# Kernel tuning notes

Measured on AMD Instinct MI355X. Metric: run time of the kernel, lower is better.

Reference implementation:

```python
import jax, jax.numpy as jnp
import numpy as np

HID = 5120
NH = 40
HD = HID // NH  # 128
S = 2048        # q_len == model_max_length (prefill)


def setup_inputs() -> dict:
    key = jax.random.key(0)
    k1, k2, k3 = jax.random.split(key, 3)
    hidden_states = jax.random.normal(k1, (1, S, HID), dtype=jnp.float32)
    W_pack_w = jax.random.normal(k2, (3 * HID, HID), dtype=jnp.float32) * 0.02
    o_proj_w = jax.random.normal(k3, (HID, HID), dtype=jnp.float32) * 0.02
    k_cache = jnp.zeros((1, NH, S, HD), dtype=jnp.float32)
    v_cache = jnp.zeros((1, NH, S, HD), dtype=jnp.float32)
    input_pos = jnp.arange(S, dtype=jnp.int32)
    # persistent causal mask [bsz, 1, max_len, max_len]; True = attend
    attention_mask = jnp.tril(jnp.ones((S, S), dtype=bool))[None, None, :, :]
    return {
        "hidden_states": hidden_states,
        "W_pack_w": W_pack_w,
        "o_proj_w": o_proj_w,
        "k_cache": k_cache,
        "v_cache": v_cache,
        "input_pos": input_pos,
        "attention_mask": attention_mask,
    }


def reference(hidden_states, W_pack_w, o_proj_w, k_cache, v_cache, input_pos, attention_mask):
    bsz, q_len, _ = hidden_states.shape
    # fused QKV projection (torch Linear weight is [out, in])
    proj = jnp.einsum("bsh,oh->bso", hidden_states, W_pack_w)  # [1,S,3H]
    q, k, v = jnp.split(proj, 3, axis=-1)
    def to_heads(t):
        return t.reshape(bsz, q_len, NH, HD).transpose(0, 2, 1, 3)  # [1,NH,S,HD]
    q, k, v = to_heads(q), to_heads(k), to_heads(v)
    # KV-cache scatter update at input_pos
    k_cache = k_cache.at[:, :, input_pos, :].set(k)
    v_cache = v_cache.at[:, :, input_pos, :].set(v)
    # s_len = input_pos[-1] + 1 == S (full prefill, static shape)
    keys = k_cache  # [1,NH,S,HD]
    vals = v_cache
    mask = attention_mask[:, :, input_pos, :]  # [1,1,S,S]
    scale = 1.0 / jnp.sqrt(jnp.asarray(HD, dtype=q.dtype))
    scores = jnp.einsum("bhqd,bhkd->bhqk", q, keys) * scale  # [1,NH,S,S]
    neg = jnp.finfo(scores.dtype).min
    scores = jnp.where(mask, scores, neg)
    attn = jax.nn.softmax(scores, axis=-1)
    out = jnp.einsum("bhqk,bhkd->bhqd", attn, vals)  # [1,NH,S,HD]
    out = out.transpose(0, 2, 1, 3).reshape(bsz, q_len, HID)
    return jnp.einsum("bsh,oh->bso", out, o_proj_w)
```

## Files before the change

### kernel.cpp

```cpp
#include <hip/hip_runtime.h>

#define S 2048
#define HID 5120
#define NH 40
#define HD 128

typedef unsigned short u16;
typedef __attribute__((ext_vector_type(8))) short short8;
typedef __attribute__((ext_vector_type(4))) float f32x4;

__device__ __forceinline__ u16 f2bf(float f) {
  union { float f; unsigned u; } x; x.f = f;
  unsigned r = x.u + 0x7fffu + ((x.u >> 16) & 1u);
  return (u16)(r >> 16);
}

__device__ __forceinline__ void gl_lds16(const void* g, void* l) {
  __builtin_amdgcn_global_load_lds((__attribute__((address_space(1))) void*)g,
                                   (__attribute__((address_space(3))) void*)l,
                                   16, 0, 0);
}

__global__ __launch_bounds__(256) void cvt4(const float4* __restrict__ s,
                                            ushort4* __restrict__ d, int n4) {
  int i = blockIdx.x * 256 + threadIdx.x;
  if (i >= n4) return;
  float4 v = s[i];
  ushort4 o;
  o.x = f2bf(v.x); o.y = f2bf(v.y); o.z = f2bf(v.z); o.w = f2bf(v.w);
  d[i] = o;
}

__global__ __launch_bounds__(512, 2) void gemm256(
    const u16* __restrict__ A, const u16* __restrict__ B,
    int N, int K,
    float* __restrict__ C,
    u16* __restrict__ qb, u16* __restrict__ kb, u16* __restrict__ vtb,
    int mode)
{
  __shared__ __align__(16) u16 As[2][16384];
  __shared__ __align__(16) u16 Bs[2][16384];

  const int tid = threadIdx.x;
  const int lane = tid & 63;
  const int wave = tid >> 6;
  const int wm = wave >> 2, wn = wave & 3;
  const int l16 = lane & 15, quad = lane >> 4;

  const int xcd = blockIdx.x & 7;
  const int j = blockIdx.x >> 3;
  const int ntile = xcd + ((j >> 3) << 3);
  if (ntile >= (N >> 8)) return;
  const int m0 = (j & 7) << 8;
  const int n0 = ntile << 8;

  const int srow = wave * 8 + (lane >> 3);
  const int scb  = (lane & 7) ^ ((lane >> 3) & 7);
  const u16* Abase = A + (long)(m0 + srow) * K + scb * 8;
  const u16* Bbase = B + (long)(n0 + srow) * K + scb * 8;
  u16* AsW = &As[0][0] + wave * 512;
  u16* BsW = &Bs[0][0] + wave * 512;

  const u16* ArBase = &As[0][0] + (wm * 128 + l16) * 64;
  const u16* BrBase = &Bs[0][0] + (wn * 64 + l16) * 64;
  const int acb0 = ((quad) ^ (l16 & 7)) * 8;
  const int acb1 = ((4 + quad) ^ (l16 & 7)) * 8;

  f32x4 acc[8][4];
#pragma unroll
  for (int i = 0; i < 8; ++i)
#pragma unroll
    for (int j2 = 0; j2 < 4; ++j2) acc[i][j2] = (f32x4){0.f, 0.f, 0.f, 0.f};

  short8 aP[2][2], aN[2][2], brg[4][2];

  const int nt = K >> 6;

#define STAGE_A(bufi, h, kt) do {                                         \
    const u16* g_ = Abase + (long)(h) * 128 * K + (long)(kt) * 64;        \
    gl_lds16(g_,           AsW + (bufi) * 16384 + (h) * 8192);            \
    gl_lds16(g_ + 64L * K, AsW + (bufi) * 16384 + (h) * 8192 + 4096);     \
  } while (0)

#define STAGE_B(bufi, h, kt) do {                                         \
    const u16* g_ = Bbase + (long)(h) * 128 * K + (long)(kt) * 64;        \
    gl_lds16(g_,           BsW + (bufi) * 16384 + (h) * 8192);            \
    gl_lds16(g_ + 64L * K, BsW + (bufi) * 16384 + (h) * 8192 + 4096);     \
  } while (0)

#define RD_A(dst, bufi, q) do {                                           \
    const u16* p_ = ArBase + (bufi) * 16384 + (q) * 2048;                 \
    dst[0][0] = *(const short8*)(p_ + acb0);                              \
    dst[0][1] = *(const short8*)(p_ + acb1);                              \
    dst[1][0] = *(const short8*)(p_ + 1024 + acb0);                       \
    dst[1][1] = *(const short8*)(p_ + 1024 + acb1);                       \
  } while (0)

#define RD_B(bufi) do {                                                   \
    const u16* p_ = BrBase + (bufi) * 16384;                              \
    brg[0][0] = *(const short8*)(p_ + acb0);                              \
    brg[0][1] = *(const short8*)(p_ + acb1);                              \
    brg[1][0] = *(const short8*)(p_ + 1024 + acb0);                       \
    brg[1][1] = *(const short8*)(p_ + 1024 + acb1);                       \
    brg[2][0] = *(const short8*)(p_ + 2048 + acb0);                       \
    brg[2][1] = *(const short8*)(p_ + 2048 + acb1);                       \
    brg[3][0] = *(const short8*)(p_ + 3072 + acb0);                       \
    brg[3][1] = *(const short8*)(p_ + 3072 + acb1);                       \
  } while (0)

#define MFMA1(mi, jj, ar) do {                                                            \
    acc[mi][jj] = __builtin_amdgcn_mfma_f32_16x16x32_bf16(ar[0], brg[jj][0], acc[mi][jj], 0, 0, 0); \
    acc[mi][jj] = __builtin_amdgcn_mfma_f32_16x16x32_bf16(ar[1], brg[jj][1], acc[mi][jj], 0, 0, 0); \
  } while (0)

#define MFMA_Q(q, a) do {                                                 \
    MFMA1((q)*2 + 0, 0, a[0]); MFMA1((q)*2 + 0, 1, a[0]);                 \
    MFMA1((q)*2 + 0, 2, a[0]); MFMA1((q)*2 + 0, 3, a[0]);                 \
    MFMA1((q)*2 + 1, 0, a[1]); MFMA1((q)*2 + 1, 1, a[1]);                 \
    MFMA1((q)*2 + 1, 2, a[1]); MFMA1((q)*2 + 1, 3, a[1]);                 \
  } while (0)

#define ASM_VMCNT(n) asm volatile("s_waitcnt vmcnt(" #n ")" ::: "memory")
#define BAR() __builtin_amdgcn_s_barrier()
#define PRIO1 __builtin_amdgcn_s_setprio(1)
#define PRIO0 __builtin_amdgcn_s_setprio(0)

#define KGROUP(S1, S2, VMN) do {                                          \
    const int bi = t & 1, bn = bi ^ 1;                                    \
                                                                 \
    RD_B(bi);                                                             \
    RD_A(aN, bi, 1);                                                      \
    if (S1) STAGE_A(bn, 1, t + 1);                                        \
    BAR();                                                                \
    PRIO1; MFMA_Q(0, aP); PRIO0;                                          \
    BAR();                                                                \
                                                                 \
    RD_A(aP, bi, 2);                                                      \
    if (S2) STAGE_B(bi, 0, t + 2);                                        \
    BAR();                                                                \
    PRIO1; MFMA_Q(1, aN); PRIO0;                                          \
    BAR();                                                                \
                                                                 \
    RD_A(aN, bi, 3);                                                      \
    if (S2) STAGE_B(bi, 1, t + 2);                                        \
    BAR();                                                                \
    PRIO1; MFMA_Q(2, aP); PRIO0;                                          \
    BAR();                                                                \
                                                                 \
    ASM_VMCNT(VMN);                                                       \
    __builtin_amdgcn_sched_barrier(0);                                    \
    BAR();                                                                \
    if (S1) RD_A(aP, bn, 0);                                              \
    PRIO1; MFMA_Q(3, aN); PRIO0;                                          \
    if (S2) STAGE_A(bi, 0, t + 2);                                        \
    BAR();                                                                \
  } while (0)

  STAGE_A(0, 0, 0); STAGE_A(0, 1, 0);
  STAGE_B(0, 0, 0); STAGE_B(0, 1, 0);
  STAGE_B(1, 0, 1); STAGE_B(1, 1, 1);
  ASM_VMCNT(4);
  __builtin_amdgcn_sched_barrier(0);
  BAR();
  STAGE_A(1, 0, 1);
  RD_A(aP, 0, 0);

  for (int t = 0; t < nt - 2; ++t) { KGROUP(1, 1, 4); }
  { int t = nt - 2; KGROUP(1, 0, 0); }
  { int t = nt - 1; KGROUP(0, 0, 0); }

  if (mode == 0) {
#pragma unroll
    for (int mi = 0; mi < 8; ++mi)
#pragma unroll
      for (int r = 0; r < 4; ++r) {
        int row = m0 + wm * 128 + mi * 16 + quad * 4 + r;
        float* cp = C + (long)row * N + n0 + wn * 64 + l16;
#pragma unroll
        for (int jj = 0; jj < 4; ++jj) cp[jj * 16] = acc[mi][jj][r];
      }
  } else {
    const int which = n0 / HID;
    const int hbase = (n0 % HID) >> 7;
    const float qs = 0.08838834764831845f;
#pragma unroll
    for (int mi = 0; mi < 8; ++mi)
#pragma unroll
      for (int jj = 0; jj < 4; ++jj) {
        int colIn = wn * 64 + jj * 16 + l16;
        int head = hbase + (colIn >> 7);
        int d = colIn & 127;
#pragma unroll
        for (int r = 0; r < 4; ++r) {
          int sI = m0 + wm * 128 + mi * 16 + quad * 4 + r;
          float v = acc[mi][jj][r];
          if (which == 0)      qb[((long)head * S + sI) * HD + d] = f2bf(v * qs);
          else if (which == 1) kb[((long)head * S + sI) * HD + d] = f2bf(v);
          else                 vtb[((long)head * HD + d) * S + sI] = f2bf(v);
        }
      }
  }

#undef STAGE_A
#undef STAGE_B
#undef RD_A
#undef RD_B
#undef MFMA1
#undef MFMA_Q
#undef ASM_VMCNT
#undef BAR
#undef PRIO1
#undef PRIO0
#undef KGROUP
}

__global__ __launch_bounds__(256) void attn_kernel(
    const u16* __restrict__ qg, const u16* __restrict__ kg,
    const u16* __restrict__ vg, u16* __restrict__ og)
{
  __shared__ __align__(16) u16 Qs[64 * 128];
  __shared__ __align__(16) u16 Ks[64 * 128];
  __shared__ __align__(16) u16 Vs[128 * 64];
  __shared__ float redm[2][64];
  __shared__ float reds[2][64];

  const int tid = threadIdx.x;
  const int lane = tid & 63;
  const int wid = tid >> 6;
  const int wm = wid >> 1, wn = wid & 1;
  const int l16 = lane & 15, quad = lane >> 4;
  const int qt = blockIdx.x;
  const int h = blockIdx.y;
  const int q0 = qt * 64;

  u16* Ps = Ks;

  {
    const u16* src = qg + ((long)h * S + q0) * HD;
#pragma unroll
    for (int cc = 0; cc < 4; ++cc) {
      int c = wid * 4 + cc;
      int row = c * 4 + (lane >> 4);
      int cb = (lane & 15) ^ (row & 7);
      gl_lds16(src + row * HD + cb * 8, &Qs[c * 512]);
    }
  }

  f32x4 acc_o[2][4];
#pragma unroll
  for (int i = 0; i < 2; ++i)
#pragma unroll
    for (int j = 0; j < 4; ++j)
      acc_o[i][j] = (f32x4){0.f, 0.f, 0.f, 0.f};
  float m_st[2][4], l_st[2][4];
#pragma unroll
  for (int i = 0; i < 2; ++i)
#pragma unroll
    for (int r = 0; r < 4; ++r) { m_st[i][r] = -1e30f; l_st[i][r] = 0.f; }

  for (int kt = 0; kt <= qt; ++kt) {
    __syncthreads();
    {
      const u16* ksrc = kg + ((long)h * S + kt * 64) * HD;
#pragma unroll
      for (int cc = 0; cc < 4; ++cc) {
        int c = wid * 4 + cc;
        int row = c * 4 + (lane >> 4);
        int cb = (lane & 15) ^ (row & 7);
        gl_lds16(ksrc + row * HD + cb * 8, &Ks[c * 512]);
      }
      const u16* vsrc = vg + (long)h * HD * S + kt * 64;
#pragma unroll
      for (int cc = 0; cc < 4; ++cc) {
        int c = wid * 4 + cc;
        int row = c * 8 + (lane >> 3);
        int cb = (lane & 7) ^ (row & 7);
        gl_lds16(vsrc + (long)row * S + cb * 8, &Vs[c * 512]);
      }
    }
    __syncthreads();

    f32x4 acc_s[2][2];
#pragma unroll
    for (int i = 0; i < 2; ++i)
#pragma unroll
      for (int j = 0; j < 2; ++j)
        acc_s[i][j] = (f32x4){0.f, 0.f, 0.f, 0.f};
#pragma unroll
    for (int kk = 0; kk < 128; kk += 32) {
      short8 aq[2], bk[2];
      const int cb0 = (kk >> 3) + quad;
#pragma unroll
      for (int i = 0; i < 2; ++i) {
        int row = wm * 32 + i * 16 + l16;
        aq[i] = *(const short8*)&Qs[row * 128 + (cb0 ^ (row & 7)) * 8];
      }
#pragma unroll
      for (int j = 0; j < 2; ++j) {
        int row = wn * 32 + j * 16 + l16;
        bk[j] = *(const short8*)&Ks[row * 128 + (cb0 ^ (row & 7)) * 8];
      }
#pragma unroll
      for (int i = 0; i < 2; ++i)
#pragma unroll
        for (int j = 0; j < 2; ++j)
          acc_s[i][j] = __builtin_amdgcn_mfma_f32_16x16x32_bf16(aq[i], bk[j], acc_s[i][j], 0, 0, 0);
    }

    if (kt == qt) {
#pragma unroll
      for (int i = 0; i < 2; ++i)
#pragma unroll
        for (int j = 0; j < 2; ++j)
#pragma unroll
          for (int r = 0; r < 4; ++r) {
            int row = wm * 32 + i * 16 + quad * 4 + r;
            int col = wn * 32 + j * 16 + l16;
            if (col > row) acc_s[i][j][r] = -1e30f;
          }
    }

#pragma unroll
    for (int i = 0; i < 2; ++i)
#pragma unroll
      for (int r = 0; r < 4; ++r) {
        float v = fmaxf(acc_s[i][0][r], acc_s[i][1][r]);
        v = fmaxf(v, __shfl_xor(v, 1));
        v = fmaxf(v, __shfl_xor(v, 2));
        v = fmaxf(v, __shfl_xor(v, 4));
        v = fmaxf(v, __shfl_xor(v, 8));
        if (l16 == 0) redm[wn][wm * 32 + i * 16 + quad * 4 + r] = v;
      }
    __syncthreads();

    float alpha[2][4], mnew[2][4], psum[2][4];
#pragma unroll
    for (int i = 0; i < 2; ++i)
#pragma unroll
      for (int r = 0; r < 4; ++r) {
        int row = wm * 32 + i * 16 + quad * 4 + r;
        float mn = fmaxf(m_st[i][r], fmaxf(redm[0][row], redm[1][row]));
        mnew[i][r] = mn;
        alpha[i][r] = __expf(m_st[i][r] - mn);
        m_st[i][r] = mn;
        psum[i][r] = 0.f;
      }
#pragma unroll
    for (int i = 0; i < 2; ++i)
#pragma unroll
      for (int j = 0; j < 2; ++j)
#pragma unroll
        for (int r = 0; r < 4; ++r) {
          int row = wm * 32 + i * 16 + quad * 4 + r;
          int col = wn * 32 + j * 16 + l16;
          float p = __expf(acc_s[i][j][r] - mnew[i][r]);
          psum[i][r] += p;
          Ps[row * 64 + ((col >> 3) ^ (row & 7)) * 8 + (col & 7)] = f2bf(p);
        }
#pragma unroll
    for (int i = 0; i < 2; ++i)
#pragma unroll
      for (int r = 0; r < 4; ++r) {
        float v = psum[i][r];
        v += __shfl_xor(v, 1);
        v += __shfl_xor(v, 2);
        v += __shfl_xor(v, 4);
        v += __shfl_xor(v, 8);
        if (l16 == 0) reds[wn][wm * 32 + i * 16 + quad * 4 + r] = v;
      }
    __syncthreads();

#pragma unroll
    for (int i = 0; i < 2; ++i)
#pragma unroll
      for (int r = 0; r < 4; ++r) {
        int row = wm * 32 + i * 16 + quad * 4 + r;
        l_st[i][r] = alpha[i][r] * l_st[i][r] + reds[0][row] + reds[1][row];
#pragma unroll
        for (int j = 0; j < 4; ++j)
          acc_o[i][j][r] *= alpha[i][r];
      }
#pragma unroll
    for (int kk = 0; kk < 64; kk += 32) {
      short8 ap[2], bv[4];
      const int cb0 = (kk >> 3) + quad;
#pragma unroll
      for (int i = 0; i < 2; ++i) {
        int m = wm * 32 + i * 16 + l16;
        ap[i] = *(const short8*)&Ps[m * 64 + (cb0 ^ (m & 7)) * 8];
      }
#pragma unroll
      for (int j = 0; j < 4; ++j) {
        int n = wn * 64 + j * 16 + l16;
        bv[j] = *(const short8*)&Vs[n * 64 + (cb0 ^ (n & 7)) * 8];
      }
#pragma unroll
      for (int i = 0; i < 2; ++i)
#pragma unroll
        for (int j = 0; j < 4; ++j)
          acc_o[i][j] = __builtin_amdgcn_mfma_f32_16x16x32_bf16(ap[i], bv[j], acc_o[i][j], 0, 0, 0);
    }
  }

#pragma unroll
  for (int i = 0; i < 2; ++i)
#pragma unroll
    for (int r = 0; r < 4; ++r) {
      int row = wm * 32 + i * 16 + quad * 4 + r;
      float inv = 1.f / l_st[i][r];
#pragma unroll
      for (int j = 0; j < 4; ++j) {
        int d = wn * 64 + j * 16 + l16;
        og[(long)(q0 + row) * HID + h * HD + d] = f2bf(acc_o[i][j][r] * inv);
      }
    }
}

extern "C" void kernel_launch(void* const* d_in, const int* in_sizes, int n_in,
                              void* d_out, int out_size, void* d_ws, size_t ws_size,
                              hipStream_t stream) {
  const float* hs = (const float*)d_in[0];
  const float* wp = (const float*)d_in[1];
  const float* wo = (const float*)d_in[2];
  float* out = (float*)d_out;
  char* ws = (char*)d_ws;

  u16* hsb = (u16*)(ws);
  u16* wpb = (u16*)(ws + 20971520L);
  u16* wob = (u16*)(ws + 178257920L);
  u16* qb  = (u16*)(ws + 230686720L);
  u16* kb  = (u16*)(ws + 251658240L);
  u16* vtb = (u16*)(ws + 272629760L);
  u16* aob = (u16*)(ws + 293601280L);
  if (ws_size < 314572800UL) return;

  cvt4<<<10240, 256, 0, stream>>>((const float4*)hs, (ushort4*)hsb, 2621440);
  cvt4<<<76800, 256, 0, stream>>>((const float4*)wp, (ushort4*)wpb, 19660800);
  cvt4<<<25600, 256, 0, stream>>>((const float4*)wo, (ushort4*)wob, 6553600);

  gemm256<<<dim3(512), dim3(512), 0, stream>>>(hsb, wpb, 15360, 5120,
                                               nullptr, qb, kb, vtb, 1);
  attn_kernel<<<dim3(32, 40), 256, 0, stream>>>(qb, kb, vtb, aob);
  gemm256<<<dim3(192), dim3(512), 0, stream>>>(aob, wob, 5120, 5120,
                                               out, nullptr, nullptr, nullptr, 0);
}
```

Measured before the change: 1.541 ms.

## Restructure attention to 128-row tiles with per-wave rows and double-buffered K/V

The attention kernel moves from 64-query tiles on 4 waves to 128-query tiles on 8 waves. Each wave owns 16 full query rows, so the row max and row sum now reduce inside the wave and the shared-memory reductions and two barriers per step are gone. Q fragments are held in registers, K/V tiles are double-buffered in one shared pool with prefetch two tiles ahead, and blocks start with the longest causal rows first to balance load. The risks are higher register and LDS pressure per block, and the loop has no explicit wait for the prefetched K/V loads, so correctness depends on the barrier draining them.

```diff
diff --git a/kernel.cpp b/kernel.cpp
--- a/kernel.cpp
+++ b/kernel.cpp
@@ -214,206 +214,188 @@
 #undef KGROUP
 }
 
-__global__ __launch_bounds__(256) void attn_kernel(
+__device__ __forceinline__ void stage_kv(const u16* __restrict__ ksrc0,
+                                         const u16* __restrict__ vsrc0,
+                                         u16* pool, int buf, int t,
+                                         int wave, int lane) {
+  const u16* ks_ = ksrc0 + (long)t * 64 * HD;
+  const u16* vs_ = vsrc0 + t * 64;
+#pragma unroll
+  for (int cc = 0; cc < 2; ++cc) {
+    int c = wave * 2 + cc;
+    int row = c * 4 + (lane >> 4);
+    int cb = (lane & 15) ^ (row & 7);
+    gl_lds16(ks_ + row * HD + cb * 8, &pool[buf * 8192 + c * 512]);
+  }
+#pragma unroll
+  for (int cc = 0; cc < 2; ++cc) {
+    int c = wave * 2 + cc;
+    int row = c * 8 + (lane >> 3);
+    int cb = (lane & 7) ^ (row & 7);
+    gl_lds16(vs_ + (long)row * S + cb * 8, &pool[16384 + buf * 8192 + c * 512]);
+  }
+}
+
+__global__ __launch_bounds__(512, 4) void attn_kernel(
     const u16* __restrict__ qg, const u16* __restrict__ kg,
     const u16* __restrict__ vg, u16* __restrict__ og)
 {
-  __shared__ __align__(16) u16 Qs[64 * 128];
-  __shared__ __align__(16) u16 Ks[64 * 128];
-  __shared__ __align__(16) u16 Vs[128 * 64];
-  __shared__ float redm[2][64];
-  __shared__ float reds[2][64];
+  __shared__ __align__(16) u16 pool[40960];
 
   const int tid = threadIdx.x;
   const int lane = tid & 63;
-  const int wid = tid >> 6;
-  const int wm = wid >> 1, wn = wid & 1;
+  const int wave = tid >> 6;
   const int l16 = lane & 15, quad = lane >> 4;
-  const int qt = blockIdx.x;
+  const int qt = (int)gridDim.x - 1 - (int)blockIdx.x;
   const int h = blockIdx.y;
-  const int q0 = qt * 64;
-
-  u16* Ps = Ks;
+  const int q0 = qt * 128;
+  const int nkt = 2 * qt + 2;
+
+  u16* Qs = pool;
+  u16* Ps = pool + 32768;
 
   {
     const u16* src = qg + ((long)h * S + q0) * HD;
 #pragma unroll
     for (int cc = 0; cc < 4; ++cc) {
-      int c = wid * 4 + cc;
+      int c = wave * 4 + cc;
       int row = c * 4 + (lane >> 4);
       int cb = (lane & 15) ^ (row & 7);
       gl_lds16(src + row * HD + cb * 8, &Qs[c * 512]);
     }
   }
-
-  f32x4 acc_o[2][4];
-#pragma unroll
-  for (int i = 0; i < 2; ++i)
-#pragma unroll
-    for (int j = 0; j < 4; ++j)
-      acc_o[i][j] = (f32x4){0.f, 0.f, 0.f, 0.f};
-  float m_st[2][4], l_st[2][4];
-#pragma unroll
-  for (int i = 0; i < 2; ++i)
-#pragma unroll
-    for (int r = 0; r < 4; ++r) { m_st[i][r] = -1e30f; l_st[i][r] = 0.f; }
-
-  for (int kt = 0; kt <= qt; ++kt) {
-    __syncthreads();
-    {
-      const u16* ksrc = kg + ((long)h * S + kt * 64) * HD;
-#pragma unroll
-      for (int cc = 0; cc < 4; ++cc) {
-        int c = wid * 4 + cc;
-        int row = c * 4 + (lane >> 4);
-        int cb = (lane & 15) ^ (row & 7);
-        gl_lds16(ksrc + row * HD + cb * 8, &Ks[c * 512]);
+  __syncthreads();
+  short8 aq[4];
+  {
+    const int row = wave * 16 + l16;
+    const u16* qr = &Qs[row * 128];
+    const int sw = row & 7;
+#pragma unroll
+    for (int ks = 0; ks < 4; ++ks)
+      aq[ks] = *(const short8*)(qr + ((ks * 4 + quad) ^ sw) * 8);
+  }
+  __syncthreads();
+
+  const u16* ksrc0 = kg + (long)h * S * HD;
+  const u16* vsrc0 = vg + (long)h * HD * S;
+
+  stage_kv(ksrc0, vsrc0, pool, 0, 0, wave, lane);
+  stage_kv(ksrc0, vsrc0, pool, 1, 1, wave, lane);
+  asm volatile("s_waitcnt vmcnt(4)" ::: "memory");
+  __builtin_amdgcn_sched_barrier(0);
+  __builtin_amdgcn_s_barrier();
+
+  f32x4 acc_o[8];
+#pragma unroll
+  for (int j2 = 0; j2 < 8; ++j2) acc_o[j2] = (f32x4){0.f, 0.f, 0.f, 0.f};
+  float m_st[4], l_st[4];
+#pragma unroll
+  for (int r = 0; r < 4; ++r) { m_st[r] = -1e30f; l_st[r] = 0.f; }
+
+  const int prow = wave * 16 + quad * 4;
+  const int rowA = wave * 16 + l16;
+  const int swA = rowA & 7;
+
+  for (int t = 0; t < nkt; ++t) {
+    const int cur = t & 1;
+    const u16* Ks = &pool[cur * 8192];
+    const u16* Vs = &pool[16384 + cur * 8192];
+
+    f32x4 acc_s[4];
+#pragma unroll
+    for (int j2 = 0; j2 < 4; ++j2) acc_s[j2] = (f32x4){0.f, 0.f, 0.f, 0.f};
+#pragma unroll
+    for (int ks = 0; ks < 4; ++ks) {
+      short8 bk[4];
+#pragma unroll
+      for (int j2 = 0; j2 < 4; ++j2) {
+        int row = j2 * 16 + l16;
+        bk[j2] = *(const short8*)&Ks[row * 128 + (((ks * 4 + quad) ^ (row & 7)) * 8)];
       }
-      const u16* vsrc = vg + (long)h * HD * S + kt * 64;
-#pragma unroll
-      for (int cc = 0; cc < 4; ++cc) {
-        int c = wid * 4 + cc;
-        int row = c * 8 + (lane >> 3);
-        int cb = (lane & 7) ^ (row & 7);
-        gl_lds16(vsrc + (long)row * S + cb * 8, &Vs[c * 512]);
+      __builtin_amdgcn_s_setprio(1);
+#pragma unroll
+      for (int j2 = 0; j2 < 4; ++j2)
+        acc_s[j2] = __builtin_amdgcn_mfma_f32_16x16x32_bf16(aq[ks], bk[j2], acc_s[j2], 0, 0, 0);
+      __builtin_amdgcn_s_setprio(0);
+    }
+
+    if (t >= nkt - 2) {
+#pragma unroll
+      for (int j2 = 0; j2 < 4; ++j2)
+#pragma unroll
+        for (int r = 0; r < 4; ++r) {
+          int row_abs = q0 + prow + r;
+          int col_abs = t * 64 + j2 * 16 + l16;
+          if (col_abs > row_abs) acc_s[j2][r] = -1e30f;
+        }
+    }
+
+    float mnew[4], alpha[4], psum[4];
+#pragma unroll
+    for (int r = 0; r < 4; ++r) {
+      float v = fmaxf(fmaxf(acc_s[0][r], acc_s[1][r]), fmaxf(acc_s[2][r], acc_s[3][r]));
+      v = fmaxf(v, __shfl_xor(v, 1));
+      v = fmaxf(v, __shfl_xor(v, 2));
+      v = fmaxf(v, __shfl_xor(v, 4));
+      v = fmaxf(v, __shfl_xor(v, 8));
+      float mn = fmaxf(m_st[r], v);
+      mnew[r] = mn;
+      alpha[r] = __expf(m_st[r] - mn);
+      m_st[r] = mn;
+      psum[r] = 0.f;
+    }
+#pragma unroll
+    for (int j2 = 0; j2 < 4; ++j2)
+#pragma unroll
+      for (int r = 0; r < 4; ++r) {
+        int row = prow + r;
+        int colL = j2 * 16 + l16;
+        float p = __expf(acc_s[j2][r] - mnew[r]);
+        psum[r] += p;
+        Ps[row * 64 + (((colL >> 3) ^ (row & 7)) * 8) + (colL & 7)] = f2bf(p);
       }
-    }
-    __syncthreads();
-
-    f32x4 acc_s[2][2];
-#pragma unroll
-    for (int i = 0; i < 2; ++i)
-#pragma unroll
-      for (int j = 0; j < 2; ++j)
-        acc_s[i][j] = (f32x4){0.f, 0.f, 0.f, 0.f};
-#pragma unroll
-    for (int kk = 0; kk < 128; kk += 32) {
-      short8 aq[2], bk[2];
-      const int cb0 = (kk >> 3) + quad;
-#pragma unroll
-      for (int i = 0; i < 2; ++i) {
-        int row = wm * 32 + i * 16 + l16;
-        aq[i] = *(const short8*)&Qs[row * 128 + (cb0 ^ (row & 7)) * 8];
+#pragma unroll
+    for (int r = 0; r < 4; ++r) {
+      float v = psum[r];
+      v += __shfl_xor(v, 1);
+      v += __shfl_xor(v, 2);
+      v += __shfl_xor(v, 4);
+      v += __shfl_xor(v, 8);
+      l_st[r] = alpha[r] * l_st[r] + v;
+#pragma unroll
+      for (int j2 = 0; j2 < 8; ++j2) acc_o[j2][r] *= alpha[r];
+    }
+
+#pragma unroll
+    for (int ks = 0; ks < 2; ++ks) {
+      short8 ap = *(const short8*)&Ps[rowA * 64 + (((ks * 4 + quad) ^ swA) * 8)];
+      short8 bv[8];
+#pragma unroll
+      for (int j2 = 0; j2 < 8; ++j2) {
+        int d = j2 * 16 + l16;
+        bv[j2] = *(const short8*)&Vs[d * 64 + (((ks * 4 + quad) ^ (d & 7)) * 8)];
       }
-#pragma unroll
-      for (int j = 0; j < 2; ++j) {
-        int row = wn * 32 + j * 16 + l16;
-        bk[j] = *(const short8*)&Ks[row * 128 + (cb0 ^ (row & 7)) * 8];
-      }
-#pragma unroll
-      for (int i = 0; i < 2; ++i)
-#pragma unroll
-        for (int j = 0; j < 2; ++j)
-          acc_s[i][j] = __builtin_amdgcn_mfma_f32_16x16x32_bf16(aq[i], bk[j], acc_s[i][j], 0, 0, 0);
-    }
-
-    if (kt == qt) {
-#pragma unroll
-      for (int i = 0; i < 2; ++i)
-#pragma unroll
-        for (int j = 0; j < 2; ++j)
-#pragma unroll
-          for (int r = 0; r < 4; ++r) {
-            int row = wm * 32 + i * 16 + quad * 4 + r;
-            int col = wn * 32 + j * 16 + l16;
-            if (col > row) acc_s[i][j][r] = -1e30f;
-          }
-    }
-
-#pragma unroll
-    for (int i = 0; i < 2; ++i)
-#pragma unroll
-      for (int r = 0; r < 4; ++r) {
-        float v = fmaxf(acc_s[i][0][r], acc_s[i][1][r]);
-        v = fmaxf(v, __shfl_xor(v, 1));
-        v = fmaxf(v, __shfl_xor(v, 2));
-        v = fmaxf(v, __shfl_xor(v, 4));
-        v = fmaxf(v, __shfl_xor(v, 8));
-        if (l16 == 0) redm[wn][wm * 32 + i * 16 + quad * 4 + r] = v;
-      }
-    __syncthreads();
-
-    float alpha[2][4], mnew[2][4], psum[2][4];
-#pragma unroll
-    for (int i = 0; i < 2; ++i)
-#pragma unroll
-      for (int r = 0; r < 4; ++r) {
-        int row = wm * 32 + i * 16 + quad * 4 + r;
-        float mn = fmaxf(m_st[i][r], fmaxf(redm[0][row], redm[1][row]));
-        mnew[i][r] = mn;
-        alpha[i][r] = __expf(m_st[i][r] - mn);
-        m_st[i][r] = mn;
-        psum[i][r] = 0.f;
-      }
-#pragma unroll
-    for (int i = 0; i < 2; ++i)
-#pragma unroll
-      for (int j = 0; j < 2; ++j)
-#pragma unroll
-        for (int r = 0; r < 4; ++r) {
-          int row = wm * 32 + i * 16 + quad * 4 + r;
-          int col = wn * 32 + j * 16 + l16;
-          float p = __expf(acc_s[i][j][r] - mnew[i][r]);
-          psum[i][r] += p;
-          Ps[row * 64 + ((col >> 3) ^ (row & 7)) * 8 + (col & 7)] = f2bf(p);
-        }
-#pragma unroll
-    for (int i = 0; i < 2; ++i)
-#pragma unroll
-      for (int r = 0; r < 4; ++r) {
-        float v = psum[i][r];
-        v += __shfl_xor(v, 1);
-        v += __shfl_xor(v, 2);
-        v += __shfl_xor(v, 4);
-        v += __shfl_xor(v, 8);
-        if (l16 == 0) reds[wn][wm * 32 + i * 16 + quad * 4 + r] = v;
-      }
-    __syncthreads();
-
-#pragma unroll
-    for (int i = 0; i < 2; ++i)
-#pragma unroll
-      for (int r = 0; r < 4; ++r) {
-        int row = wm * 32 + i * 16 + quad * 4 + r;
-        l_st[i][r] = alpha[i][r] * l_st[i][r] + reds[0][row] + reds[1][row];
-#pragma unroll
-        for (int j = 0; j < 4; ++j)
-          acc_o[i][j][r] *= alpha[i][r];
-      }
-#pragma unroll
-    for (int kk = 0; kk < 64; kk += 32) {
-      short8 ap[2], bv[4];
-      const int cb0 = (kk >> 3) + quad;
-#pragma unroll
-      for (int i = 0; i < 2; ++i) {
-        int m = wm * 32 + i * 16 + l16;
-        ap[i] = *(const short8*)&Ps[m * 64 + (cb0 ^ (m & 7)) * 8];
-      }
-#pragma unroll
-      for (int j = 0; j < 4; ++j) {
-        int n = wn * 64 + j * 16 + l16;
-        bv[j] = *(const short8*)&Vs[n * 64 + (cb0 ^ (n & 7)) * 8];
-      }
-#pragma unroll
-      for (int i = 0; i < 2; ++i)
-#pragma unroll
-        for (int j = 0; j < 4; ++j)
-          acc_o[i][j] = __builtin_amdgcn_mfma_f32_16x16x32_bf16(ap[i], bv[j], acc_o[i][j], 0, 0, 0);
-    }
-  }
-
-#pragma unroll
-  for (int i = 0; i < 2; ++i)
-#pragma unroll
-    for (int r = 0; r < 4; ++r) {
-      int row = wm * 32 + i * 16 + quad * 4 + r;
-      float inv = 1.f / l_st[i][r];
-#pragma unroll
-      for (int j = 0; j < 4; ++j) {
-        int d = wn * 64 + j * 16 + l16;
-        og[(long)(q0 + row) * HID + h * HD + d] = f2bf(acc_o[i][j][r] * inv);
-      }
-    }
+      __builtin_amdgcn_s_setprio(1);
+#pragma unroll
+      for (int j2 = 0; j2 < 8; ++j2)
+        acc_o[j2] = __builtin_amdgcn_mfma_f32_16x16x32_bf16(ap, bv[j2], acc_o[j2], 0, 0, 0);
+      __builtin_amdgcn_s_setprio(0);
+    }
+
+    if (t + 1 < nkt) {
+      __syncthreads();
+      if (t + 2 < nkt) stage_kv(ksrc0, vsrc0, pool, cur, t + 2, wave, lane);
+    }
+  }
+
+#pragma unroll
+  for (int r = 0; r < 4; ++r) {
+    float inv = 1.f / l_st[r];
+    u16* op = og + (long)(q0 + prow + r) * HID + h * HD + l16;
+#pragma unroll
+    for (int j2 = 0; j2 < 8; ++j2)
+      op[j2 * 16] = f2bf(acc_o[j2][r] * inv);
+  }
 }
 
 extern "C" void kernel_launch(void* const* d_in, const int* in_sizes, int n_in,
@@ -440,7 +422,7 @@
 
   gemm256<<<dim3(512), dim3(512), 0, stream>>>(hsb, wpb, 15360, 5120,
                                                nullptr, qb, kb, vtb, 1);
-  attn_kernel<<<dim3(32, 40), 256, 0, stream>>>(qb, kb, vtb, aob);
+  attn_kernel<<<dim3(16, 40), 512, 0, stream>>>(qb, kb, vtb, aob);
   gemm256<<<dim3(192), dim3(512), 0, stream>>>(aob, wob, 5120, 5120,
                                                out, nullptr, nullptr, nullptr, 0);
 }
```

New measurement: 1.474 ms. 4.3% less time.
